# Optimization experiments

Hardware: AMD Instinct MI355X
Metric: run time of the kernel (lower is better)

## Reference

```python
import jax, jax.numpy as jnp
import numpy as np

TAU = 3.0      # time horizon (init arg tau)
FIX = 0.2      # correction gain (init arg fix)


def setup_inputs() -> dict:
    key = jax.random.key(0)
    k1, k2, k3, k4, k5 = jax.random.split(key, 5)
    B, N, K = 256, 1024, 32
    p_cur = jax.random.normal(k1, (B, N, 2), dtype=jnp.float32) * 10.0   # positions (meters)
    v_cur = jax.random.normal(k2, (B, N, 2), dtype=jnp.float32)          # previous velocities
    v_desire = jax.random.normal(k3, (B, N, 2), dtype=jnp.float32)       # desired velocities
    near_ped_idx = jax.random.randint(k4, (B, N, K), 0, N, dtype=jnp.int32)
    neigh_ped_mask = jax.random.randint(k5, (B, N, K), 0, 2).astype(jnp.float32)
    return {
        "p_cur": p_cur,
        "v_cur": v_cur,
        "v_desire": v_desire,
        "near_ped_idx": near_ped_idx,
        "neigh_ped_mask": neigh_ped_mask,
        "collision_threshold": 1,
    }


def reference(p_cur, v_cur, v_desire, near_ped_idx, neigh_ped_mask, collision_threshold):
    # Gather neighbor positions/velocities: (B,N,K,2). vmap over batch avoids
    # materializing the (B,N,N,2) expanded tensor the torch code logically builds.
    gather = jax.vmap(lambda arr, idx: arr[idx])
    neighbors_pos = gather(p_cur, near_ped_idx)
    neighbors_vel = gather(v_cur, near_ped_idx)

    mask = neigh_ped_mask[..., None]                      # (B,N,K,1)
    neighbors_pos = neighbors_pos * mask
    neighbors_vel = neighbors_vel * mask

    rel_pos = p_cur[:, :, None, :] - neighbors_pos        # (B,N,K,2)
    rel_vel = v_desire[:, :, None, :] - neighbors_vel     # (B,N,K,2)

    dot_pos_vel = jnp.sum(rel_pos * rel_vel, axis=-1)     # (B,N,K)
    dot_vel_vel = jnp.sum(rel_vel * rel_vel, axis=-1) + 1e-6
    t_min = dot_pos_vel / (dot_vel_vel + 1e-6)
    t_min = jnp.where(jnp.isnan(t_min), TAU, t_min)
    t_clamp = jnp.clip(t_min, 0.0, TAU)

    min_dist = jnp.linalg.norm(rel_pos + t_clamp[..., None] * rel_vel, axis=-1)
    min_dist = jnp.where(jnp.isnan(min_dist), 1e6, min_dist)

    collision_mask = (min_dist < collision_threshold) & (neigh_ped_mask != 0)

    # 90-degree rotated rel_pos as collision normal
    normal = jnp.stack([-rel_pos[..., 1], rel_pos[..., 0]], axis=-1)   # (B,N,K,2)
    denom = jnp.linalg.norm(normal, axis=-1, keepdims=True)
    normal = jnp.where(collision_mask[..., None], normal / (denom + 1e-6), 0.0)

    correction = jnp.sum(normal, axis=2)                  # (B,N,2)
    correction = jnp.nan_to_num(correction, nan=0.0)
    v_next = v_desire + correction * FIX
    return v_next
```

## Files before the change

kernel.cpp:

```cpp
#include <hip/hip_runtime.h>

#define TAU 3.0f
#define FIX 0.2f
#define NPED 1024
#define PEDS_PER_BLOCK 256
#define BLOCK 512
#define GROUPS (BLOCK / 8)
#define PASSES (PEDS_PER_BLOCK / GROUPS)

__global__ __launch_bounds__(BLOCK) void rvo_kernel(
    const float* __restrict__ p_cur,
    const float* __restrict__ v_cur,
    const float* __restrict__ v_desire,
    const int*   __restrict__ near_idx,
    const float* __restrict__ mask_arr,
    const int*   __restrict__ cth,
    float*       __restrict__ out,
    int N)
{
    __shared__ float2 tpos[NPED];
    __shared__ float2 tvel[NPED];

    const int tid    = threadIdx.x;
    const int bpb    = N / PEDS_PER_BLOCK;
    const int batch  = blockIdx.x / bpb;
    const int pbase  = (blockIdx.x % bpb) * PEDS_PER_BLOCK;

    const float2* pb2 = (const float2*)(p_cur) + (size_t)batch * N;
    const float2* vb2 = (const float2*)(v_cur) + (size_t)batch * N;
    #pragma unroll
    for (int n = tid; n < NPED; n += BLOCK) {
        tpos[n] = pb2[n];
        tvel[n] = vb2[n];
    }
    __syncthreads();

    const float thr2 = (float)cth[0] * (float)cth[0];

    const int sub  = tid & 7;
    const int pgrp = tid >> 3;

    #pragma unroll
    for (int pass = 0; pass < PASSES; ++pass) {
        const int ped  = pbase + pass * GROUPS + pgrp;
        const size_t pair = (size_t)batch * N + ped;

        const float2 self = tpos[ped];
        const float2 vd   = ((const float2*)v_desire)[pair];
        const float px = self.x, py = self.y;
        const float vdx = vd.x, vdy = vd.y;

        const int4   i4 = ((const int4*)near_idx)[pair * 8 + sub];
        const float4 m4 = ((const float4*)mask_arr)[pair * 8 + sub];
        const int   idxs[4] = {i4.x, i4.y, i4.z, i4.w};
        const float ms[4]   = {m4.x, m4.y, m4.z, m4.w};

        float nx = 0.0f, ny = 0.0f;
        #pragma unroll
        for (int j = 0; j < 4; ++j) {
            const float2 nbp = tpos[idxs[j]];
            const float2 nbv = tvel[idxs[j]];
            const float m = ms[j];
            const float rpx = fmaf(-m, nbp.x, px);
            const float rpy = fmaf(-m, nbp.y, py);
            const float rvx = fmaf(-m, nbv.x, vdx);
            const float rvy = fmaf(-m, nbv.y, vdy);

            const float dpv = fmaf(rpx, rvx, rpy * rvy);
            const float dvv = fmaf(rvx, rvx, fmaf(rvy, rvy, 2e-6f));
            float t = dpv * __builtin_amdgcn_rcpf(dvv);
            t = fminf(fmaxf(t, 0.0f), TAU);

            const float cx = fmaf(t, rvx, rpx);
            const float cy = fmaf(t, rvy, rpy);
            const float md2 = fmaf(cx, cx, cy * cy);

            const float s = fmaf(rpx, rpx, rpy * rpy);
            const float sel0 = (s > 0.0f) ? __builtin_amdgcn_rsqf(s) : 0.0f;
            const float w    = (md2 < thr2) ? m : 0.0f;
            const float sel  = sel0 * w;
            nx = fmaf(-rpy, sel, nx);
            ny = fmaf( rpx, sel, ny);
        }

        #pragma unroll
        for (int d = 4; d > 0; d >>= 1) {
            nx += __shfl_down(nx, d, 8);
            ny += __shfl_down(ny, d, 8);
        }

        if (sub == 0) {
            ((float2*)out)[pair] = make_float2(fmaf(nx, FIX, vdx),
                                               fmaf(ny, FIX, vdy));
        }
    }
}

extern "C" void kernel_launch(void* const* d_in, const int* in_sizes, int n_in,
                              void* d_out, int out_size, void* d_ws, size_t ws_size,
                              hipStream_t stream) {
    const float* p_cur    = (const float*)d_in[0];
    const float* v_cur    = (const float*)d_in[1];
    const float* v_desire = (const float*)d_in[2];
    const int*   near_idx = (const int*)d_in[3];
    const float* mask_arr = (const float*)d_in[4];
    const int*   cth      = (const int*)d_in[5];
    float*       out      = (float*)d_out;

    const int N  = NPED;
    const int BN = in_sizes[0] / 2;
    dim3 block(BLOCK);
    dim3 grid(BN / PEDS_PER_BLOCK);
    rvo_kernel<<<grid, block, 0, stream>>>(p_cur, v_cur, v_desire, near_idx,
                                           mask_arr, cth, out, N);
}
```

Measured before the change: 105.8 us.

## Prefetch next-pass neighbor data, pack pos/vel in LDS, use DPP reduction

Loads the neighbor indices, masks and desired velocity for the next pass while the current pass computes, using nontemporal loads, so global-load latency overlaps with compute. Position and velocity are packed into one float4 shared array, so each neighbor needs a single LDS read instead of two. The 8-lane shuffle reduction becomes DPP row-shift adds, and launch bounds request higher occupancy. This uses more registers for the prefetched values, which the occupancy hint may constrain.

```diff
diff --git a/kernel.cpp b/kernel.cpp
--- a/kernel.cpp
+++ b/kernel.cpp
@@ -8,7 +8,18 @@
 #define GROUPS (BLOCK / 8)
 #define PASSES (PEDS_PER_BLOCK / GROUPS)
 
-__global__ __launch_bounds__(BLOCK) void rvo_kernel(
+typedef int   v4i __attribute__((ext_vector_type(4)));
+typedef float v4f __attribute__((ext_vector_type(4)));
+
+template <int CTRL>
+__device__ __forceinline__ float dpp_shl_add(float x) {
+    union { float f; int i; } s, r;
+    s.f = x;
+    r.i = __builtin_amdgcn_update_dpp(0, s.i, CTRL, 0xF, 0xF, true);
+    return x + r.f;
+}
+
+__global__ __launch_bounds__(BLOCK, 8) void rvo_kernel(
     const float* __restrict__ p_cur,
     const float* __restrict__ v_cur,
     const float* __restrict__ v_desire,
@@ -18,8 +29,7 @@
     float*       __restrict__ out,
     int N)
 {
-    __shared__ float2 tpos[NPED];
-    __shared__ float2 tvel[NPED];
+    __shared__ float4 tpv[NPED];
 
     const int tid    = threadIdx.x;
     const int bpb    = N / PEDS_PER_BLOCK;
@@ -30,8 +40,9 @@
     const float2* vb2 = (const float2*)(v_cur) + (size_t)batch * N;
     #pragma unroll
     for (int n = tid; n < NPED; n += BLOCK) {
-        tpos[n] = pb2[n];
-        tvel[n] = vb2[n];
+        const float2 p = pb2[n];
+        const float2 v = vb2[n];
+        tpv[n] = make_float4(p.x, p.y, v.x, v.y);
     }
     __syncthreads();
 
@@ -40,31 +51,45 @@
     const int sub  = tid & 7;
     const int pgrp = tid >> 3;
 
+    const v4i*    idxv = (const v4i*)near_idx;
+    const v4f*    mskv = (const v4f*)mask_arr;
+    const float2* vdv  = (const float2*)v_desire;
+
+    size_t pair = (size_t)batch * N + (pbase + pgrp);
+
+    v4i    i4 = __builtin_nontemporal_load(&idxv[pair * 8 + sub]);
+    v4f    m4 = __builtin_nontemporal_load(&mskv[pair * 8 + sub]);
+    float2 vd = vdv[pair];
+
     #pragma unroll
     for (int pass = 0; pass < PASSES; ++pass) {
-        const int ped  = pbase + pass * GROUPS + pgrp;
-        const size_t pair = (size_t)batch * N + ped;
+        v4i ni4; v4f nm4; float2 nvd;
+        if (pass + 1 < PASSES) {
+            const size_t np = pair + GROUPS;
+            ni4 = __builtin_nontemporal_load(&idxv[np * 8 + sub]);
+            nm4 = __builtin_nontemporal_load(&mskv[np * 8 + sub]);
+            nvd = vdv[np];
+        } else {
+            ni4 = i4; nm4 = m4; nvd = vd;
+        }
 
-        const float2 self = tpos[ped];
-        const float2 vd   = ((const float2*)v_desire)[pair];
+        const int ped = pbase + pass * GROUPS + pgrp;
+        const float4 self = tpv[ped];
         const float px = self.x, py = self.y;
         const float vdx = vd.x, vdy = vd.y;
 
-        const int4   i4 = ((const int4*)near_idx)[pair * 8 + sub];
-        const float4 m4 = ((const float4*)mask_arr)[pair * 8 + sub];
         const int   idxs[4] = {i4.x, i4.y, i4.z, i4.w};
         const float ms[4]   = {m4.x, m4.y, m4.z, m4.w};
 
         float nx = 0.0f, ny = 0.0f;
         #pragma unroll
         for (int j = 0; j < 4; ++j) {
-            const float2 nbp = tpos[idxs[j]];
-            const float2 nbv = tvel[idxs[j]];
+            const float4 nb = tpv[idxs[j]];
             const float m = ms[j];
-            const float rpx = fmaf(-m, nbp.x, px);
-            const float rpy = fmaf(-m, nbp.y, py);
-            const float rvx = fmaf(-m, nbv.x, vdx);
-            const float rvy = fmaf(-m, nbv.y, vdy);
+            const float rpx = fmaf(-m, nb.x, px);
+            const float rpy = fmaf(-m, nb.y, py);
+            const float rvx = fmaf(-m, nb.z, vdx);
+            const float rvy = fmaf(-m, nb.w, vdy);
 
             const float dpv = fmaf(rpx, rvx, rpy * rvy);
             const float dvv = fmaf(rvx, rvx, fmaf(rvy, rvy, 2e-6f));
@@ -83,16 +108,20 @@
             ny = fmaf( rpx, sel, ny);
         }
 
-        #pragma unroll
-        for (int d = 4; d > 0; d >>= 1) {
-            nx += __shfl_down(nx, d, 8);
-            ny += __shfl_down(ny, d, 8);
-        }
+        nx = dpp_shl_add<0x104>(nx);
+        nx = dpp_shl_add<0x102>(nx);
+        nx = dpp_shl_add<0x101>(nx);
+        ny = dpp_shl_add<0x104>(ny);
+        ny = dpp_shl_add<0x102>(ny);
+        ny = dpp_shl_add<0x101>(ny);
 
         if (sub == 0) {
             ((float2*)out)[pair] = make_float2(fmaf(nx, FIX, vdx),
                                                fmaf(ny, FIX, vdy));
         }
+
+        pair += GROUPS;
+        i4 = ni4; m4 = nm4; vd = nvd;
     }
 }
 
```

Result: slower. 116.7 us (+10.3%).
